# Performance work log

Measured on AMD Instinct MI355X. Metric: run time of the kernel, lower is better.

Reference implementation:

```python
import jax, jax.numpy as jnp
import numpy as np

MAX_S, MIN_S, MAX_R = 3.0, 0.5, 3.0
A = (MAX_S - MIN_S) / 2.0   # 1.25
B = (MAX_S + MIN_S) / 2.0   # 1.75
C = (MAX_R - 1.0) / 2.0     # 1.0
D = (MAX_R + 1.0) / 2.0     # 2.0

# 3x3 kernel base points, row-major: dim0 = dy, dim1 = dx, shape [2, 9]
BASE = jnp.array([[-1, -1], [-1, 0], [-1, 1], [0, -1], [0, 0], [0, 1],
                  [1, -1], [1, 0], [1, 1]], dtype=jnp.float32).T


def conv2d(x, w, b=None):
    y = jax.lax.conv_general_dilated(x, w, window_strides=(1, 1),
                                     padding=((1, 1), (1, 1)),
                                     dimension_numbers=('NCHW', 'OIHW', 'NCHW'))
    if b is not None:
        y = y + b[None, :, None, None]
    return y


def setup_inputs() -> dict:
    key = jax.random.key(0)
    ks = jax.random.split(key, 8)
    return {
        'x': jax.random.normal(ks[0], (8, 64, 128, 128), jnp.float32),
        'w_main': jax.random.normal(ks[1], (64, 64, 3, 3), jnp.float32) * 0.05,
        'w_rot': jax.random.normal(ks[2], (2, 64, 3, 3), jnp.float32) * 0.05,
        'b_rot': jax.random.normal(ks[3], (2,), jnp.float32) * 0.05,
        'w_str': jax.random.normal(ks[4], (1, 64, 3, 3), jnp.float32) * 0.05,
        'b_str': jax.random.normal(ks[5], (1,), jnp.float32) * 0.05,
        'w_whl': jax.random.normal(ks[6], (1, 64, 3, 3), jnp.float32) * 0.05,
        'b_whl': jax.random.normal(ks[7], (1,), jnp.float32) * 0.05,
    }


def reference(x, w_main, w_rot, b_rot, w_str, b_str, w_whl, b_whl):
    b, c, H, W = x.shape
    K = 9
    # --- offset generation ---
    rot = conv2d(x, w_rot, b_rot)                     # [b,2,H,W]
    sin, cos = rot[:, 0], rot[:, 1]
    norm = jnp.sqrt(sin ** 2 + cos ** 2 + 1e-6)
    sin, cos = sin / norm, cos / norm
    r = jnp.tanh(conv2d(x, w_str, b_str))[:, 0] * A + B   # [b,H,W]
    wr = jnp.tanh(conv2d(x, w_whl, b_whl))[:, 0] * C + D  # [b,H,W]
    ky, kx = BASE[0], BASE[1]                             # [9]
    kyb = ky[None, :, None, None]
    kxb = kx[None, :, None, None]
    o0 = kyb * (wr * r)[:, None]                          # [b,9,H,W]
    o1 = kxb * wr[:, None]
    sinb, cosb = sin[:, None], cos[:, None]
    dy = cosb * o0 + sinb * o1 - kyb                      # rotation then subtract base
    dx = -sinb * o0 + cosb * o1 - kxb
    # --- deformable sampling positions (stride=1, pad=1, dil=1) ---
    py = jnp.arange(H, dtype=x.dtype)[None, None, :, None] + kyb + dy  # [b,9,H,W]
    px = jnp.arange(W, dtype=x.dtype)[None, None, None, :] + kxb + dx
    y0f = jnp.floor(py); x0f = jnp.floor(px)
    ly = py - y0f; lx = px - x0f
    y0 = y0f.astype(jnp.int32); x0 = x0f.astype(jnp.int32)
    x_flat = x.reshape(b, c, H * W)

    def gather(yi, xi, wgt):
        valid = (yi >= 0) & (yi < H) & (xi >= 0) & (xi < W)
        idx = jnp.clip(yi, 0, H - 1) * W + jnp.clip(xi, 0, W - 1)
        g = jnp.take_along_axis(x_flat, idx.reshape(b, 1, -1), axis=2)
        g = g.reshape(b, c, K, H, W)
        return g * (wgt * valid)[:, None]

    val = (gather(y0, x0, (1 - ly) * (1 - lx))
           + gather(y0, x0 + 1, (1 - ly) * lx)
           + gather(y0 + 1, x0, ly * (1 - lx))
           + gather(y0 + 1, x0 + 1, ly * lx))          # [b,c,9,H,W]
    # final 3x3 conv over sampled points == contraction over (c, k)
    out = jnp.einsum('bckhw,ock->bohw', val, w_main.reshape(w_main.shape[0], c, K))
    return out
```

## Files before the change

kernel.cpp:

```cpp
#include <hip/hip_runtime.h>
#include <hip/hip_bf16.h>
#include <hip/hip_fp16.h>
#include <math.h>

#define HH 128
#define WW 128
#define HWSZ (HH*WW)
#define CH 64
#define OC 64
#define NB 8
#define RG 28
#define RPX (RG*RG)

#define XT_BYTES   (16777216u)
#define OFFS_BYTES (2097152u)

typedef _Float16 f16x8 __attribute__((ext_vector_type(8)));
typedef __attribute__((ext_vector_type(4))) float f32x4_t;

__global__ __launch_bounds__(256) void pre_kernel(
    const float* __restrict__ x, const float* __restrict__ w_main,
    const float* __restrict__ w_rot, const float* __restrict__ w_str,
    const float* __restrict__ w_whl,
    const float* __restrict__ b_rot, const float* __restrict__ b_str,
    const float* __restrict__ b_whl,
    __half* __restrict__ xT, __half* __restrict__ wmT2,
    float4* __restrict__ offs)
{
    __shared__ float shmem[64 * 65];
    const int t = threadIdx.x;
    const int i = blockIdx.x;

    if (i >= 2560) {
        const int base = (i - 2560) * 4096 + t * 16;
        #pragma unroll
        for (int j = 0; j < 16; ++j) {
            const int e = base + j;
            const int k = e >> 12;
            const int r = e & 4095;
            const int o = r >> 6;
            const int c = r & 63;
            wmT2[e] = __float2half(w_main[(size_t)o * (CH * 9) + c * 9 + k]);
        }
        return;
    }

    if (i >= 512) {
        float (*tile)[65] = (float(*)[65])shmem;
        const int it = i - 512;
        const int b = it & 7;
        const int j = it >> 3;
        const int h  = j >> 1;
        const int w0 = (j & 1) * 64;
        const float* xb = x + (size_t)b * CH * HWSZ + h * WW + w0;
        {
            const int w = t & 63, c0 = (t >> 6) * 16;
            #pragma unroll
            for (int jj = 0; jj < 16; ++jj)
                tile[c0 + jj][w] = xb[(size_t)(c0 + jj) * HWSZ + w];
        }
        __syncthreads();
        {
            const int c = t & 63, wq = t >> 6;
            __half* o = xT + ((size_t)b * HWSZ + h * WW + w0) * 64;
            #pragma unroll
            for (int jj = 0; jj < 16; ++jj) {
                const int w = wq * 16 + jj;
                o[(size_t)w * 64 + c] = __float2half(tile[c][w]);
            }
        }
        return;
    }

    float (*xs)[4][WW] = (float(*)[4][WW])shmem;
    const int b  = i & 7;
    const int rp = i >> 3;
    const int h0 = rp * 2;
    const float* xb = x + (size_t)b * CH * HWSZ;
    const int r = t >> 7, w = t & 127;
    const int wl = max(w - 1, 0), wr2 = min(w + 1, WW - 1);
    const float ml = (w > 0) ? 1.f : 0.f, mr = (w < WW - 1) ? 1.f : 0.f;
    float a0 = 0.f, a1 = 0.f, a2 = 0.f, a3 = 0.f;

    for (int cg = 0; cg < 8; ++cg) {
        const int c0 = cg * 8;
        __syncthreads();
        #pragma unroll
        for (int jj = 0; jj < 4; ++jj) {
            const int u   = t + jj * 256;
            const int ch  = u >> 7;
            const int rem = u & 127;
            const int row = rem >> 5;
            const int w4  = (rem & 31) * 4;
            const int grow = h0 - 1 + row;
            float4 v = make_float4(0.f, 0.f, 0.f, 0.f);
            if (grow >= 0 && grow < HH)
                v = *(const float4*)&xb[((size_t)(c0 + ch) * HH + grow) * WW + w4];
            *(float4*)&xs[ch][row][w4] = v;
        }
        __syncthreads();
        #pragma unroll
        for (int ch = 0; ch < 8; ++ch) {
            const int cc = c0 + ch;
            #pragma unroll
            for (int dy = 0; dy < 3; ++dy) {
                const float* row_ = &xs[ch][r + dy][0];
                const float nl = row_[wl] * ml;
                const float nc = row_[w];
                const float nr = row_[wr2] * mr;
                const int d0 = cc * 9 + dy * 3;
                a0 = fmaf(nl, w_rot[d0 + 0], a0); a0 = fmaf(nc, w_rot[d0 + 1], a0); a0 = fmaf(nr, w_rot[d0 + 2], a0);
                a1 = fmaf(nl, w_rot[576 + d0 + 0], a1); a1 = fmaf(nc, w_rot[576 + d0 + 1], a1); a1 = fmaf(nr, w_rot[576 + d0 + 2], a1);
                a2 = fmaf(nl, w_str[d0 + 0], a2); a2 = fmaf(nc, w_str[d0 + 1], a2); a2 = fmaf(nr, w_str[d0 + 2], a2);
                a3 = fmaf(nl, w_whl[d0 + 0], a3); a3 = fmaf(nc, w_whl[d0 + 1], a3); a3 = fmaf(nr, w_whl[d0 + 2], a3);
            }
        }
    }

    float sv = a0 + b_rot[0], cv = a1 + b_rot[1];
    const float inv = 1.0f / sqrtf(sv * sv + cv * cv + 1e-6f);
    const float rr = tanhf(a2 + b_str[0]) * 1.25f + 1.75f;
    const float wq = tanhf(a3 + b_whl[0]) * 1.0f + 2.0f;
    offs[(size_t)b * HWSZ + (h0 + r) * WW + w] = make_float4(sv * inv, cv * inv, wq * rr, wq);
}

__global__ __launch_bounds__(256, 3) void deform_kernel(
    const __half* __restrict__ xT, const __half* __restrict__ wmT2,
    const float4* __restrict__ offs, float* __restrict__ out)
{
    __shared__ union {
        uint4 xs[RPX * 4];
        float ots[64][67];
    } sh;
    const int t  = threadIdx.x;
    const int wv = t >> 6;
    const int l  = t & 63;
    const int lm = l & 15;
    const int lg = l >> 4;
    const int i  = blockIdx.x;
    const int b  = i & 7;
    const int tile = i >> 3;
    const int w0 = (tile & 15) * 8;
    const int h0 = (tile >> 4) * 8;
    const int pi = wv * 16 + lm;
    const int h = h0 + (pi >> 3);
    const int w = w0 + (pi & 7);
    const float4 o4 = offs[(size_t)b * HWSZ + h * WW + w];
    const float sv = o4.x, cv = o4.y, av = o4.z, wvl = o4.w;
    const float hh  = (float)h;
    const float wwf = (float)w;
    const __half* xb = xT + (size_t)b * HWSZ * 64;

    int ti[9], td[9];
    __half2 w2[9][4];
    #pragma unroll
    for (int k = 0; k < 9; ++k) {
        const float kyf = (float)(k / 3) - 1.f;
        const float kxf = (float)(k % 3) - 1.f;
        const float o0v = kyf * av;
        const float o1v = kxf * wvl;
        const float pyf = hh  + cv * o0v + sv * o1v;
        const float pxf = wwf - sv * o0v + cv * o1v;
        const float y0f = floorf(pyf), x0f = floorf(pxf);
        const float ly = pyf - y0f, lx = pxf - x0f;
        const int y0 = (int)y0f, x0i = (int)x0f;
        const int y1 = y0 + 1, x1 = x0i + 1;
        const bool vy0 = (y0 >= 0) && (y0 < HH);
        const bool vy1 = (y1 >= 0) && (y1 < HH);
        const bool vx0 = (x0i >= 0) && (x0i < WW);
        const bool vx1 = (x1 >= 0) && (x1 < WW);
        w2[k][0] = __float2half2_rn((1.f - ly) * (1.f - lx) * ((vy0 && vx0) ? 1.f : 0.f));
        w2[k][1] = __float2half2_rn((1.f - ly) * lx         * ((vy0 && vx1) ? 1.f : 0.f));
        w2[k][2] = __float2half2_rn(ly * (1.f - lx)         * ((vy1 && vx0) ? 1.f : 0.f));
        w2[k][3] = __float2half2_rn(ly * lx                 * ((vy1 && vx1) ? 1.f : 0.f));
        const int iy0 = min(max(y0, 0), HH - 1), iy1 = min(max(y1, 0), HH - 1);
        const int ix0 = min(max(x0i, 0), WW - 1), ix1 = min(max(x1, 0), WW - 1);
        ti[k] = (iy0 - (h0 - 10)) * RG + (ix0 - (w0 - 10));
        td[k] = (ix1 - ix0) | ((iy1 - iy0) << 1);
    }

    f32x4_t acc0 = {0.f, 0.f, 0.f, 0.f};
    f32x4_t acc1 = acc0, acc2 = acc0, acc3 = acc0;

    for (int g = 0; g < 2; ++g) {
        __syncthreads();
        for (int u = t; u < RPX * 4; u += 256) {
            const int pxu = u >> 2, q = u & 3;
            const int lr = pxu / RG;
            const int lc = pxu - lr * RG;
            const int gy = min(max(h0 - 10 + lr, 0), HH - 1);
            const int gx = min(max(w0 - 10 + lc, 0), WW - 1);
            sh.xs[pxu * 4 + (q ^ ((pxu >> 1) & 3))] =
                *(const uint4*)(xb + (size_t)(gy * WW + gx) * 64 + g * 32 + q * 8);
        }
        __syncthreads();
        const int cb0 = g * 32 + lg * 8;
        #pragma unroll
        for (int k = 0; k < 9; ++k) {
            const int i00 = ti[k];
            const int dxx = td[k] & 1;
            const int dyy = (td[k] >> 1) * RG;
            const int i01 = i00 + dxx;
            const int i10 = i00 + dyy;
            const int i11 = i10 + dxx;
            union Q { uint4 q; __half2 h2[4]; };
            Q q00, q01, q10, q11;
            q00.q = sh.xs[i00 * 4 + (lg ^ ((i00 >> 1) & 3))];
            q01.q = sh.xs[i01 * 4 + (lg ^ ((i01 >> 1) & 3))];
            q10.q = sh.xs[i10 * 4 + (lg ^ ((i10 >> 1) & 3))];
            q11.q = sh.xs[i11 * 4 + (lg ^ ((i11 >> 1) & 3))];
            union { __half2 h2[4]; f16x8 v; } af;
            #pragma unroll
            for (int j = 0; j < 4; ++j) {
                af.h2[j] = __hfma2(q00.h2[j], w2[k][0],
                           __hfma2(q01.h2[j], w2[k][1],
                           __hfma2(q10.h2[j], w2[k][2],
                           __hmul2(q11.h2[j], w2[k][3]))));
            }
            const __half* wp = wmT2 + ((size_t)k * 64 + lm) * 64 + cb0;
            const f16x8 bf0 = *(const f16x8*)(wp);
            const f16x8 bf1 = *(const f16x8*)(wp + 1024);
            const f16x8 bf2v = *(const f16x8*)(wp + 2048);
            const f16x8 bf3 = *(const f16x8*)(wp + 3072);
            acc0 = __builtin_amdgcn_mfma_f32_16x16x32_f16(af.v, bf0,  acc0, 0, 0, 0);
            acc1 = __builtin_amdgcn_mfma_f32_16x16x32_f16(af.v, bf1,  acc1, 0, 0, 0);
            acc2 = __builtin_amdgcn_mfma_f32_16x16x32_f16(af.v, bf2v, acc2, 0, 0, 0);
            acc3 = __builtin_amdgcn_mfma_f32_16x16x32_f16(af.v, bf3,  acc3, 0, 0, 0);
        }
    }

    __syncthreads();
    const int pxw = wv * 16 + lg * 4;
    #pragma unroll
    for (int rg2 = 0; rg2 < 4; ++rg2) {
        sh.ots[pxw + rg2][ 0 + lm] = acc0[rg2];
        sh.ots[pxw + rg2][16 + lm] = acc1[rg2];
        sh.ots[pxw + rg2][32 + lm] = acc2[rg2];
        sh.ots[pxw + rg2][48 + lm] = acc3[rg2];
    }
    __syncthreads();
    const int oo = t >> 2;
    const int q  = (t & 3) * 16;
    #pragma unroll
    for (int j2 = 0; j2 < 4; ++j2) {
        const int px = q + j2 * 4;
        float4 v = make_float4(sh.ots[px + 0][oo], sh.ots[px + 1][oo],
                               sh.ots[px + 2][oo], sh.ots[px + 3][oo]);
        *(float4*)&out[((size_t)b * OC + oo) * HWSZ +
                       (h0 + (px >> 3)) * WW + w0 + (px & 7)] = v;
    }
}

extern "C" void kernel_launch(void* const* d_in, const int* in_sizes, int n_in,
                              void* d_out, int out_size, void* d_ws, size_t ws_size,
                              hipStream_t stream)
{
    const float* x      = (const float*)d_in[0];
    const float* w_main = (const float*)d_in[1];
    const float* w_rot  = (const float*)d_in[2];
    const float* b_rot  = (const float*)d_in[3];
    const float* w_str  = (const float*)d_in[4];
    const float* b_str  = (const float*)d_in[5];
    const float* w_whl  = (const float*)d_in[6];
    const float* b_whl  = (const float*)d_in[7];
    float* out = (float*)d_out;

    char* ws = (char*)d_ws;
    __half*  xT   = (__half*)ws;
    float4*  offs = (float4*)(ws + XT_BYTES);
    __half*  wmT2 = (__half*)(ws + XT_BYTES + OFFS_BYTES);

    pre_kernel<<<dim3(2569), 256, 0, stream>>>(x, w_main, w_rot, w_str, w_whl,
                                               b_rot, b_str, b_whl,
                                               xT, wmT2, offs);
    deform_kernel<<<dim3(2048), 256, 0, stream>>>(xT, wmT2, offs, out);
}
```

Measured before the change: 215.0 us.

## Fuse NHWC fp16 transpose into offset-conv blocks, one row per block

Removes the separate transpose blocks that re-read x to build the fp16 channel-last copy. The offset-conv blocks now write that copy from their already staged shared-memory row. Each block handles one output row with two threads per pixel splitting the channels, and a shuffle combines the partial sums. Every input row is now loaded three times by neighbouring blocks instead of about twice, and the fp16 stores are 16-byte chunks at a 128-byte stride across pixels.

```diff
diff --git a/kernel.cpp b/kernel.cpp
--- a/kernel.cpp
+++ b/kernel.cpp
@@ -27,12 +27,12 @@
     __half* __restrict__ xT, __half* __restrict__ wmT2,
     float4* __restrict__ offs)
 {
-    __shared__ float shmem[64 * 65];
+    __shared__ float xs[3][16][WW];
     const int t = threadIdx.x;
     const int i = blockIdx.x;
 
-    if (i >= 2560) {
-        const int base = (i - 2560) * 4096 + t * 16;
+    if (i >= 1024) {
+        const int base = (i - 1024) * 4096 + t * 16;
         #pragma unroll
         for (int j = 0; j < 16; ++j) {
             const int e = base + j;
@@ -45,66 +45,49 @@
         return;
     }
 
-    if (i >= 512) {
-        float (*tile)[65] = (float(*)[65])shmem;
-        const int it = i - 512;
-        const int b = it & 7;
-        const int j = it >> 3;
-        const int h  = j >> 1;
-        const int w0 = (j & 1) * 64;
-        const float* xb = x + (size_t)b * CH * HWSZ + h * WW + w0;
-        {
-            const int w = t & 63, c0 = (t >> 6) * 16;
-            #pragma unroll
-            for (int jj = 0; jj < 16; ++jj)
-                tile[c0 + jj][w] = xb[(size_t)(c0 + jj) * HWSZ + w];
-        }
-        __syncthreads();
-        {
-            const int c = t & 63, wq = t >> 6;
-            __half* o = xT + ((size_t)b * HWSZ + h * WW + w0) * 64;
-            #pragma unroll
-            for (int jj = 0; jj < 16; ++jj) {
-                const int w = wq * 16 + jj;
-                o[(size_t)w * 64 + c] = __float2half(tile[c][w]);
-            }
-        }
-        return;
-    }
-
-    float (*xs)[4][WW] = (float(*)[4][WW])shmem;
     const int b  = i & 7;
-    const int rp = i >> 3;
-    const int h0 = rp * 2;
+    const int h0 = i >> 3;
+    const int w    = t >> 1;
+    const int half = t & 1;
     const float* xb = x + (size_t)b * CH * HWSZ;
-    const int r = t >> 7, w = t & 127;
+
     const int wl = max(w - 1, 0), wr2 = min(w + 1, WW - 1);
     const float ml = (w > 0) ? 1.f : 0.f, mr = (w < WW - 1) ? 1.f : 0.f;
     float a0 = 0.f, a1 = 0.f, a2 = 0.f, a3 = 0.f;
 
-    for (int cg = 0; cg < 8; ++cg) {
-        const int c0 = cg * 8;
-        __syncthreads();
-        #pragma unroll
-        for (int jj = 0; jj < 4; ++jj) {
+    for (int p = 0; p < 4; ++p) {
+        const int c0p = p * 16;
+        __syncthreads();
+        #pragma unroll
+        for (int jj = 0; jj < 6; ++jj) {
             const int u   = t + jj * 256;
-            const int ch  = u >> 7;
-            const int rem = u & 127;
-            const int row = rem >> 5;
-            const int w4  = (rem & 31) * 4;
+            const int row = u >> 9;
+            const int rem = u & 511;
+            const int ch  = rem >> 5;
+            const int w4  = (rem & 31) << 2;
             const int grow = h0 - 1 + row;
             float4 v = make_float4(0.f, 0.f, 0.f, 0.f);
             if (grow >= 0 && grow < HH)
-                v = *(const float4*)&xb[((size_t)(c0 + ch) * HH + grow) * WW + w4];
-            *(float4*)&xs[ch][row][w4] = v;
-        }
-        __syncthreads();
-        #pragma unroll
-        for (int ch = 0; ch < 8; ++ch) {
-            const int cc = c0 + ch;
+                v = *(const float4*)&xb[((size_t)(c0p + ch) * HH + grow) * WW + w4];
+            *(float4*)&xs[row][ch][w4] = v;
+        }
+        __syncthreads();
+
+        {
+            union { __half hx[8]; uint4 u4; } pk;
+            #pragma unroll
+            for (int j = 0; j < 8; ++j)
+                pk.hx[j] = __float2half(xs[1][half * 8 + j][w]);
+            *(uint4*)&xT[((size_t)b * HWSZ + h0 * WW + w) * 64 + c0p + half * 8] = pk.u4;
+        }
+
+        #pragma unroll
+        for (int j = 0; j < 8; ++j) {
+            const int chl = half * 8 + j;
+            const int cc  = c0p + chl;
             #pragma unroll
             for (int dy = 0; dy < 3; ++dy) {
-                const float* row_ = &xs[ch][r + dy][0];
+                const float* row_ = &xs[dy][chl][0];
                 const float nl = row_[wl] * ml;
                 const float nc = row_[w];
                 const float nr = row_[wr2] * mr;
@@ -117,11 +100,19 @@
         }
     }
 
-    float sv = a0 + b_rot[0], cv = a1 + b_rot[1];
-    const float inv = 1.0f / sqrtf(sv * sv + cv * cv + 1e-6f);
-    const float rr = tanhf(a2 + b_str[0]) * 1.25f + 1.75f;
-    const float wq = tanhf(a3 + b_whl[0]) * 1.0f + 2.0f;
-    offs[(size_t)b * HWSZ + (h0 + r) * WW + w] = make_float4(sv * inv, cv * inv, wq * rr, wq);
+    a0 += __shfl_xor(a0, 1);
+    a1 += __shfl_xor(a1, 1);
+    a2 += __shfl_xor(a2, 1);
+    a3 += __shfl_xor(a3, 1);
+
+    if (half == 0) {
+        float sv = a0 + b_rot[0], cv = a1 + b_rot[1];
+        const float inv = 1.0f / sqrtf(sv * sv + cv * cv + 1e-6f);
+        const float rr = tanhf(a2 + b_str[0]) * 1.25f + 1.75f;
+        const float wq = tanhf(a3 + b_whl[0]) * 1.0f + 2.0f;
+        offs[(size_t)b * HWSZ + h0 * WW + w] =
+            make_float4(sv * inv, cv * inv, wq * rr, wq);
+    }
 }
 
 __global__ __launch_bounds__(256, 3) void deform_kernel(
@@ -270,7 +261,7 @@
     float4*  offs = (float4*)(ws + XT_BYTES);
     __half*  wmT2 = (__half*)(ws + XT_BYTES + OFFS_BYTES);
 
-    pre_kernel<<<dim3(2569), 256, 0, stream>>>(x, w_main, w_rot, w_str, w_whl,
+    pre_kernel<<<dim3(1033), 256, 0, stream>>>(x, w_main, w_rot, w_str, w_whl,
                                                b_rot, b_str, b_whl,
                                                xT, wmT2, offs);
     deform_kernel<<<dim3(2048), 256, 0, stream>>>(xT, wmT2, offs, out);
```

Measured after the change: 230.9 us. +7.4%, slower.
